# Optimization experiments

Hardware: AMD Instinct MI355X
Metric: run time of the kernel (lower is better)

The kernel has to match this reference:

```python
import jax, jax.numpy as jnp
import numpy as np

HID = 1024
HEADS = 16
HEAD_DIM = HID // HEADS
SCALE = np.sqrt(HEAD_DIM).astype(np.float32)


def setup_inputs() -> dict:
    key = jax.random.key(0)
    ks = jax.random.split(key, 13)
    B, S = 4, 2048
    inp = {
        'query': jax.random.normal(ks[0], (B, S, HID), jnp.float32),
        'key': jax.random.normal(ks[1], (B, S, HID), jnp.float32),
        'value': jax.random.normal(ks[2], (B, S, HID), jnp.float32),
        'mask': jax.random.randint(ks[3], (B, 1, 1, S), 0, 2, jnp.int32),
        'Wq': jax.random.normal(ks[4], (HID, HID), jnp.float32) / np.sqrt(HID),
        'bq': jax.random.normal(ks[5], (HID,), jnp.float32) * 0.02,
        'Wk': jax.random.normal(ks[6], (HID, HID), jnp.float32) / np.sqrt(HID),
        'bk': jax.random.normal(ks[7], (HID,), jnp.float32) * 0.02,
        'Wv': jax.random.normal(ks[8], (HID, HID), jnp.float32) / np.sqrt(HID),
        'bv': jax.random.normal(ks[9], (HID,), jnp.float32) * 0.02,
        'Wo': jax.random.normal(ks[10], (HID, HID), jnp.float32) / np.sqrt(HID),
        'bo': jax.random.normal(ks[11], (HID,), jnp.float32) * 0.02,
    }
    return inp


def reference(query, key, value, mask, Wq, bq, Wk, bk, Wv, bv, Wo, bo):
    B, Sq, _ = query.shape
    # nn.Linear: x @ W.T + b
    Q = (query @ Wq.T + bq).reshape(B, Sq, HEADS, HEAD_DIM)
    K = (key @ Wk.T + bk).reshape(B, -1, HEADS, HEAD_DIM)
    V = (value @ Wv.T + bv).reshape(B, -1, HEADS, HEAD_DIM)
    # energy: [B, H, Q, K]
    energy = jnp.einsum('bqnh,bknh->bnqk', Q, K) / SCALE
    energy = jnp.where(mask == 0, jnp.float32(-1e10), energy)
    attention = jax.nn.softmax(energy, axis=-1)  # dropout p=0.0 -> identity
    x = jnp.einsum('bnqk,bknh->bqnh', attention, V).reshape(B, Sq, HID)
    return x @ Wo.T + bo
```

## Files before the change

kernel.cpp:

```cpp
#include <hip/hip_runtime.h>
#include <cstddef>
#include <math.h>

#define S_LEN  2048
#define HID_C  1024
#define NHEADS 16
#define HDIM   64

typedef __attribute__((ext_vector_type(8))) short bf16x8;
typedef __attribute__((ext_vector_type(4))) float f32x4;
typedef __attribute__((ext_vector_type(16))) float f32x16;
typedef unsigned short ushort_t;

#define LOG2E 1.44269504088896f

__device__ __forceinline__ unsigned short f32_to_bf16_rn(float f) {
    unsigned int u = __float_as_uint(f);
    return (unsigned short)((u + 0x8000u) >> 16);
}

__device__ __forceinline__ float fexp2(float x) {
    float r;
    asm("v_exp_f32 %0, %1" : "=v"(r) : "v"(x));
    return r;
}

__device__ __forceinline__ void gload16(const ushort_t* g, ushort_t* l) {
    __builtin_amdgcn_global_load_lds(
        (const __attribute__((address_space(1))) void*)g,
        (__attribute__((address_space(3))) void*)l, 16, 0, 0);
}

__device__ __forceinline__ float tmax16(const f32x16& v) {
    float a0 = fmaxf(v[0], v[1]),   a1 = fmaxf(v[2], v[3]);
    float a2 = fmaxf(v[4], v[5]),   a3 = fmaxf(v[6], v[7]);
    float a4 = fmaxf(v[8], v[9]),   a5 = fmaxf(v[10], v[11]);
    float a6 = fmaxf(v[12], v[13]), a7 = fmaxf(v[14], v[15]);
    float b0 = fmaxf(a0, a1), b1 = fmaxf(a2, a3);
    float b2 = fmaxf(a4, a5), b3 = fmaxf(a6, a7);
    return fmaxf(fmaxf(b0, b1), fmaxf(b2, b3));
}
__device__ __forceinline__ float tsum16(const f32x16& v) {
    float a0 = v[0] + v[1],   a1 = v[2] + v[3];
    float a2 = v[4] + v[5],   a3 = v[6] + v[7];
    float a4 = v[8] + v[9],   a5 = v[10] + v[11];
    float a6 = v[12] + v[13], a7 = v[14] + v[15];
    float b0 = a0 + a1, b1 = a2 + a3, b2 = a4 + a5, b3 = a6 + a7;
    return (b0 + b1) + (b2 + b3);
}

__global__ void scan_mask(const int* __restrict__ mask, int* __restrict__ cidx,
                          int* __restrict__ nvalid, int* __restrict__ npads) {
    const int b = blockIdx.x;
    const int lane = threadIdx.x;
    int base = 0;
    for (int i = 0; i < S_LEN / 64; ++i) {
        const int s = i * 64 + lane;
        const int v = mask[b * S_LEN + s];
        const unsigned long long bal = __ballot(v != 0);
        const int pre = __popcll(bal & ((1ull << lane) - 1ull));
        if (v) cidx[b * S_LEN + base + pre] = s;
        base += (int)__popcll(bal);
    }
    if (lane == 0) { nvalid[b] = base; npads[b] = (base + 63) & ~63; }
}

#define CONVB 12288

__global__ void prep_gather(
    const float* __restrict__ query,
    const float* __restrict__ Wq, const float* __restrict__ Wk,
    const float* __restrict__ Wo, const float* __restrict__ Wv,
    const float* __restrict__ key, const float* __restrict__ value,
    const int* __restrict__ cidx, const int* __restrict__ nvalid,
    ushort_t* __restrict__ Qbf, ushort_t* __restrict__ Wqb,
    ushort_t* __restrict__ Wkb, ushort_t* __restrict__ Wob,
    ushort_t* __restrict__ Wvb,
    ushort_t* __restrict__ Kc, ushort_t* __restrict__ Vc,
    float* __restrict__ Mbc)
{
    if (blockIdx.x < CONVB) {
        const unsigned SEG = 4u * S_LEN * HID_C;
        const unsigned NW = HID_C * HID_C;
        unsigned i = (blockIdx.x * 256u + threadIdx.x) * 4u;
        const float* src; ushort_t* dst;
        if (i < SEG) { src = query; dst = Qbf; }
        else {
            i -= SEG;
            if (i < NW) { src = Wq; dst = Wqb; }
            else { i -= NW;
                if (i < NW) { src = Wk; dst = Wkb; }
                else { i -= NW;
                    if (i < NW) { src = Wo; dst = Wob; }
                    else { i -= NW; if (i >= NW) return; src = Wv; dst = Wvb; }
                }
            }
        }
        float4 v = *reinterpret_cast<const float4*>(src + i);
        uint2 p;
        p.x = ((unsigned)f32_to_bf16_rn(v.y) << 16) | f32_to_bf16_rn(v.x);
        p.y = ((unsigned)f32_to_bf16_rn(v.w) << 16) | f32_to_bf16_rn(v.z);
        *reinterpret_cast<uint2*>(dst + i) = p;
    } else {
        const int r = blockIdx.x - CONVB;
        const int b = r >> 11, j = r & 2047;
        const int tid = threadIdx.x;
        const int nv = nvalid[b];
        if (tid == 0) Mbc[r] = (j < nv) ? 0.f : -1e30f;
        const int np128 = (nv + 127) & ~127;
        if (j >= np128) return;
        uint2* kd = reinterpret_cast<uint2*>(Kc + (size_t)r * HID_C + tid * 4);
        uint2* vd = reinterpret_cast<uint2*>(Vc + (size_t)r * HID_C + tid * 4);
        if (j < nv) {
            const int src = cidx[b * S_LEN + j];
            const float4 kv = *reinterpret_cast<const float4*>(
                key + ((size_t)b * S_LEN + src) * HID_C + tid * 4);
            const float4 vv = *reinterpret_cast<const float4*>(
                value + ((size_t)b * S_LEN + src) * HID_C + tid * 4);
            uint2 kp, vp;
            kp.x = ((unsigned)f32_to_bf16_rn(kv.y) << 16) | f32_to_bf16_rn(kv.x);
            kp.y = ((unsigned)f32_to_bf16_rn(kv.w) << 16) | f32_to_bf16_rn(kv.z);
            vp.x = ((unsigned)f32_to_bf16_rn(vv.y) << 16) | f32_to_bf16_rn(vv.x);
            vp.y = ((unsigned)f32_to_bf16_rn(vv.w) << 16) | f32_to_bf16_rn(vv.z);
            *kd = kp; *vd = vp;
        } else {
            *kd = make_uint2(0u, 0u); *vd = make_uint2(0u, 0u);
        }
    }
}

__device__ __forceinline__ void gemm_core(
    const ushort_t* __restrict__ Ab, const ushort_t* __restrict__ Wb,
    const float* __restrict__ bias, ushort_t* __restrict__ outB,
    int bm, int bn, int N, int K, float oscale, bool rowBias,
    ushort_t* Ah, ushort_t* Bh)
{
    const int tid  = threadIdx.x;
    const int lane = tid & 63;
    const int wave = tid >> 6;
    const int wm = (wave >> 1) * 64;
    const int wn = (wave & 1) * 64;
    const int fr = lane & 15;
    const int kq = lane >> 4;

    int srow[2], skq[2];
#pragma unroll
    for (int i = 0; i < 2; ++i) {
        const int s = i * 256 + tid;
        srow[i] = s >> 2;
        skq[i] = (s & 3) ^ ((s >> 3) & 3);
    }
    const int wslot = tid & 192;

    f32x4 acc[4][4];
#pragma unroll
    for (int i = 0; i < 4; ++i)
#pragma unroll
        for (int j = 0; j < 4; ++j)
#pragma unroll
            for (int r = 0; r < 4; ++r) acc[i][j][r] = 0.f;

    for (int k0 = 0; k0 < K; k0 += 32) {
        __syncthreads();
#pragma unroll
        for (int i = 0; i < 2; ++i) {
            const int sb = (i * 256 + wslot) * 8;
            gload16(Ab + (size_t)(bm + srow[i]) * K + k0 + skq[i] * 8, Ah + sb);
            gload16(Wb + (size_t)(bn + srow[i]) * K + k0 + skq[i] * 8, Bh + sb);
        }
        __syncthreads();

        bf16x8 fah[4], fbh[4];
#pragma unroll
        for (int mi = 0; mi < 4; ++mi) {
            const int rr = wm + mi * 16 + fr;
            fah[mi] = *reinterpret_cast<const bf16x8*>(
                Ah + (rr * 4 + (kq ^ ((rr >> 1) & 3))) * 8);
        }
#pragma unroll
        for (int ni = 0; ni < 4; ++ni) {
            const int rr = wn + ni * 16 + fr;
            fbh[ni] = *reinterpret_cast<const bf16x8*>(
                Bh + (rr * 4 + (kq ^ ((rr >> 1) & 3))) * 8);
        }

#pragma unroll
        for (int mi = 0; mi < 4; ++mi)
#pragma unroll
            for (int ni = 0; ni < 4; ++ni)
                acc[mi][ni] = __builtin_amdgcn_mfma_f32_16x16x32_bf16(
                    fah[mi], fbh[ni], acc[mi][ni], 0, 0, 0);
    }

    const int fq = lane >> 4;
    if (rowBias) {
#pragma unroll
        for (int mi = 0; mi < 4; ++mi)
#pragma unroll
            for (int r = 0; r < 4; ++r) {
                const int row = bm + wm + mi * 16 + fq * 4 + r;
                const float bvr = bias[row];
#pragma unroll
                for (int ni = 0; ni < 4; ++ni)
                    outB[(size_t)row * N + bn + wn + ni * 16 + fr] =
                        f32_to_bf16_rn((acc[mi][ni][r] + bvr) * oscale);
            }
    } else {
        float bv[4];
#pragma unroll
        for (int ni = 0; ni < 4; ++ni) bv[ni] = bias[bn + wn + ni * 16 + fr];
#pragma unroll
        for (int mi = 0; mi < 4; ++mi)
#pragma unroll
            for (int ni = 0; ni < 4; ++ni) {
                const size_t rowb = (size_t)(bm + wm + mi * 16 + fq * 4);
                const int col = bn + wn + ni * 16 + fr;
#pragma unroll
                for (int r = 0; r < 4; ++r)
                    outB[(rowb + r) * N + col] =
                        f32_to_bf16_rn((acc[mi][ni][r] + bv[ni]) * oscale);
            }
    }
}

__global__ __launch_bounds__(256) void proj_fused(
    const ushort_t* __restrict__ Qbf, const ushort_t* __restrict__ Kc,
    const ushort_t* __restrict__ Wvb, const ushort_t* __restrict__ Vc,
    const ushort_t* __restrict__ Wqb, const ushort_t* __restrict__ Wkb,
    const float* __restrict__ bq, const float* __restrict__ bk,
    const float* __restrict__ bv, const int* __restrict__ npads,
    ushort_t* __restrict__ Qb, ushort_t* __restrict__ Kb,
    ushort_t* __restrict__ Vtg, float sc2)
{
    __shared__ __align__(16) ushort_t Ah[128 * 32];
    __shared__ __align__(16) ushort_t Bh[128 * 32];

    int id = blockIdx.x;
    if (id < 512) {
        gemm_core(Qbf, Wqb, bq, Qb, (id >> 3) * 128, (id & 7) * 128,
                  HID_C, HID_C, sc2, false, Ah, Bh);
    } else if (id < 1024) {
        id -= 512;
        const int bm = (id >> 3) * 128;
        if ((bm & 2047) >= npads[bm >> 11]) return;
        gemm_core(Kc, Wkb, bk, Kb, bm, (id & 7) * 128,
                  HID_C, HID_C, 1.f, false, Ah, Bh);
    } else {
        id -= 1024;
        const int bn = (id & 63) * 128;
        if ((bn & 2047) >= npads[bn >> 11]) return;
        gemm_core(Wvb, Vc, bv, Vtg, (id >> 6) * 128, bn,
                  4 * S_LEN, HID_C, 1.f, true, Ah, Bh);
    }
}

__global__ __launch_bounds__(256) void gemm_out(
    const ushort_t* __restrict__ Xhi, const ushort_t* __restrict__ Xlo,
    const ushort_t* __restrict__ Wb, const float* __restrict__ bias,
    float* __restrict__ outF, int M, int N, int K)
{
    __shared__ __align__(16) ushort_t Ah[128 * 32];
    __shared__ __align__(16) ushort_t Al[128 * 32];
    __shared__ __align__(16) ushort_t Bh[128 * 32];

    const int tid  = threadIdx.x;
    const int lane = tid & 63;
    const int wave = tid >> 6;
    const int bm = blockIdx.y * 128;
    const int bn = blockIdx.x * 128;
    const int wm = (wave >> 1) * 64;
    const int wn = (wave & 1) * 64;
    const int fr = lane & 15;
    const int kq = lane >> 4;

    int srow[2], skq[2];
#pragma unroll
    for (int i = 0; i < 2; ++i) {
        const int s = i * 256 + tid;
        srow[i] = s >> 2;
        skq[i] = (s & 3) ^ ((s >> 3) & 3);
    }
    const int wslot = tid & 192;

    f32x4 acc[4][4];
#pragma unroll
    for (int i = 0; i < 4; ++i)
#pragma unroll
        for (int j = 0; j < 4; ++j)
#pragma unroll
            for (int r = 0; r < 4; ++r) acc[i][j][r] = 0.f;

    for (int k0 = 0; k0 < K; k0 += 32) {
        __syncthreads();
#pragma unroll
        for (int i = 0; i < 2; ++i) {
            const int sb = (i * 256 + wslot) * 8;
            const size_t ga = (size_t)(bm + srow[i]) * K + k0 + skq[i] * 8;
            gload16(Xhi + ga, Ah + sb);
            gload16(Xlo + ga, Al + sb);
            gload16(Wb + (size_t)(bn + srow[i]) * K + k0 + skq[i] * 8, Bh + sb);
        }
        __syncthreads();

        bf16x8 fah[4], fal[4], fbh[4];
#pragma unroll
        for (int mi = 0; mi < 4; ++mi) {
            const int rr = wm + mi * 16 + fr;
            const int sl = (rr * 4 + (kq ^ ((rr >> 1) & 3))) * 8;
            fah[mi] = *reinterpret_cast<const bf16x8*>(Ah + sl);
            fal[mi] = *reinterpret_cast<const bf16x8*>(Al + sl);
        }
#pragma unroll
        for (int ni = 0; ni < 4; ++ni) {
            const int rr = wn + ni * 16 + fr;
            fbh[ni] = *reinterpret_cast<const bf16x8*>(
                Bh + (rr * 4 + (kq ^ ((rr >> 1) & 3))) * 8);
        }

#pragma unroll
        for (int mi = 0; mi < 4; ++mi)
#pragma unroll
            for (int ni = 0; ni < 4; ++ni) {
                acc[mi][ni] = __builtin_amdgcn_mfma_f32_16x16x32_bf16(
                    fah[mi], fbh[ni], acc[mi][ni], 0, 0, 0);
                acc[mi][ni] = __builtin_amdgcn_mfma_f32_16x16x32_bf16(
                    fal[mi], fbh[ni], acc[mi][ni], 0, 0, 0);
            }
    }

    const int fq = lane >> 4;
    float bv[4];
#pragma unroll
    for (int ni = 0; ni < 4; ++ni) bv[ni] = bias[bn + wn + ni * 16 + fr];
#pragma unroll
    for (int mi = 0; mi < 4; ++mi)
#pragma unroll
        for (int ni = 0; ni < 4; ++ni) {
            const size_t rowb = (size_t)(bm + wm + mi * 16 + fq * 4);
            const int col = bn + wn + ni * 16 + fr;
#pragma unroll
            for (int r = 0; r < 4; ++r)
                outF[(rowb + r) * N + col] = acc[mi][ni][r] + bv[ni];
        }
}

#define QBLK 128
#define KVB  64
#define LDA  72

__global__ __launch_bounds__(256) void flash_attn_bf16(
    const ushort_t* __restrict__ Qb, const ushort_t* __restrict__ Kb,
    const ushort_t* __restrict__ Vtg, const float* __restrict__ maskb,
    const int* __restrict__ npads,
    ushort_t* __restrict__ Xhi, ushort_t* __restrict__ Xlo)
{
    __shared__ __align__(16) ushort_t Ks[KVB * LDA];
    __shared__ __align__(16) ushort_t Vt[HDIM * LDA];
    __shared__ float Xpose[QBLK];

    const int n  = blockIdx.x;
    const int bh = (n & 7) * 8 + ((n >> 3) & 7);
    const int qx = n >> 6;
    const int b  = bh >> 4;
    const int h  = bh & 15;
    const int q0 = qx * QBLK;

    const int tid  = threadIdx.x;
    const int lane = tid & 63;
    const int w    = tid >> 6;
    const int lq = lane & 31;
    const int lh = lane >> 5;

    const size_t bS = (size_t)b * S_LEN;
    const int hc = h * HDIM;
    const int npad = npads[b];

    bf16x8 qf[4];
#pragma unroll
    for (int s = 0; s < 4; ++s)
        qf[s] = *reinterpret_cast<const bf16x8*>(
            &Qb[(bS + q0 + w * 32 + lq) * HID_C + hc + s * 16 + lh * 8]);

    f32x16 OV[2], zc;
#pragma unroll
    for (int r = 0; r < 16; ++r) { OV[0][r] = 0.f; OV[1][r] = 0.f; zc[r] = 0.f; }
    float m_ = -1e30f, l_ = 0.f;

    const int sr  = tid >> 2;
    const int seg = tid & 3;
    const ushort_t* kbase = &Kb[(bS + sr) * HID_C + hc + seg * 16];
    const ushort_t* vbase = &Vtg[(size_t)(hc + sr) * (4 * S_LEN) + bS + seg * 16];

    {
        bf16x8 kv0 = *reinterpret_cast<const bf16x8*>(kbase);
        bf16x8 kv1 = *reinterpret_cast<const bf16x8*>(kbase + 8);
        bf16x8 vv0 = *reinterpret_cast<const bf16x8*>(vbase);
        bf16x8 vv1 = *reinterpret_cast<const bf16x8*>(vbase + 8);
        *reinterpret_cast<bf16x8*>(&Ks[sr * LDA + seg * 16])     = kv0;
        *reinterpret_cast<bf16x8*>(&Ks[sr * LDA + seg * 16 + 8]) = kv1;
        *reinterpret_cast<bf16x8*>(&Vt[sr * LDA + seg * 16])     = vv0;
        *reinterpret_cast<bf16x8*>(&Vt[sr * LDA + seg * 16 + 8]) = vv1;
        __syncthreads();
    }

    for (int t = 0; t < npad; t += KVB) {
        f32x16 S[2];
        __builtin_amdgcn_s_setprio(1);
#pragma unroll
        for (int kt = 0; kt < 2; ++kt) {
            bf16x8 kf0 = *reinterpret_cast<const bf16x8*>(
                &Ks[(kt * 32 + lq) * LDA + lh * 8]);
            S[kt] = __builtin_amdgcn_mfma_f32_32x32x16_bf16(kf0, qf[0], zc, 0, 0, 0);
#pragma unroll
            for (int s = 1; s < 4; ++s) {
                bf16x8 kf = *reinterpret_cast<const bf16x8*>(
                    &Ks[(kt * 32 + lq) * LDA + s * 16 + lh * 8]);
                S[kt] = __builtin_amdgcn_mfma_f32_32x32x16_bf16(
                    kf, qf[s], S[kt], 0, 0, 0);
            }
        }
        __builtin_amdgcn_s_setprio(0);

        const bool more = (t + KVB < npad);
        bf16x8 kv0n, kv1n, vv0n, vv1n;
        if (more) {
            const ushort_t* kp = kbase + (size_t)(t + KVB) * HID_C;
            const ushort_t* vp = vbase + (t + KVB);
            kv0n = *reinterpret_cast<const bf16x8*>(kp);
            kv1n = *reinterpret_cast<const bf16x8*>(kp + 8);
            vv0n = *reinterpret_cast<const bf16x8*>(vp);
            vv1n = *reinterpret_cast<const bf16x8*>(vp + 8);
        }

        if (!more) {
#pragma unroll
            for (int kt = 0; kt < 2; ++kt)
#pragma unroll
                for (int g = 0; g < 4; ++g) {
                    float4 mv = *reinterpret_cast<const float4*>(
                        &maskb[bS + t + kt * 32 + g * 8 + lh * 4]);
#pragma unroll
                    for (int e = 0; e < 4; ++e)
                        S[kt][g * 4 + e] += reinterpret_cast<const float*>(&mv)[e];
                }
        }

        float mx = fmaxf(tmax16(S[0]), tmax16(S[1]));
        mx = fmaxf(mx, __shfl_xor(mx, 32));

        if (!__all(mx <= m_ + 8.f)) {
            float mn = fmaxf(m_, mx);
            float corr = fexp2(m_ - mn);
            m_ = mn; l_ *= corr;
            if (lh == 0) Xpose[w * 32 + lq] = corr;
#pragma unroll
            for (int r = 0; r < 16; ++r) {
                float cq = Xpose[w * 32 + (r & 3) + 8 * (r >> 2) + 4 * lh];
                OV[0][r] *= cq;
                OV[1][r] *= cq;
            }
        }

#pragma unroll
        for (int kt = 0; kt < 2; ++kt)
#pragma unroll
            for (int r = 0; r < 16; ++r) S[kt][r] = fexp2(S[kt][r] - m_);
        float ls = tsum16(S[0]) + tsum16(S[1]);
        ls += __shfl_xor(ls, 32);
        l_ += ls;

        bf16x8 pa[4];
#pragma unroll
        for (int kt = 0; kt < 2; ++kt)
#pragma unroll
            for (int u = 0; u < 2; ++u) {
                const int bb = u * 8;
                unsigned int c0, c1, c2, c3;
                asm("v_cvt_pk_bf16_f32 %0, %1, %2"
                    : "=v"(c0) : "v"(S[kt][bb + 0]), "v"(S[kt][bb + 1]));
                asm("v_cvt_pk_bf16_f32 %0, %1, %2"
                    : "=v"(c1) : "v"(S[kt][bb + 2]), "v"(S[kt][bb + 3]));
                asm("v_cvt_pk_bf16_f32 %0, %1, %2"
                    : "=v"(c2) : "v"(S[kt][bb + 4]), "v"(S[kt][bb + 5]));
                asm("v_cvt_pk_bf16_f32 %0, %1, %2"
                    : "=v"(c3) : "v"(S[kt][bb + 6]), "v"(S[kt][bb + 7]));
                asm("v_permlane32_swap_b32 %0, %1" : "+v"(c0), "+v"(c2));
                asm("v_permlane32_swap_b32 %0, %1" : "+v"(c1), "+v"(c3));
                uint4 wv = make_uint4(c0, c1, c2, c3);
                pa[kt * 2 + u] = *reinterpret_cast<bf16x8*>(&wv);
            }

        __builtin_amdgcn_s_setprio(1);
#pragma unroll
        for (int dt = 0; dt < 2; ++dt)
#pragma unroll
            for (int f = 0; f < 4; ++f) {
                bf16x8 vf = *reinterpret_cast<const bf16x8*>(
                    &Vt[(dt * 32 + lq) * LDA + f * 16 + lh * 8]);
                OV[dt] = __builtin_amdgcn_mfma_f32_32x32x16_bf16(
                    pa[f], vf, OV[dt], 0, 0, 0);
            }
        __builtin_amdgcn_s_setprio(0);

        __syncthreads();
        if (more) {
            *reinterpret_cast<bf16x8*>(&Ks[sr * LDA + seg * 16])     = kv0n;
            *reinterpret_cast<bf16x8*>(&Ks[sr * LDA + seg * 16 + 8]) = kv1n;
            *reinterpret_cast<bf16x8*>(&Vt[sr * LDA + seg * 16])     = vv0n;
            *reinterpret_cast<bf16x8*>(&Vt[sr * LDA + seg * 16 + 8]) = vv1n;
            __syncthreads();
        }
    }

    if (lh == 0) Xpose[w * 32 + lq] = 1.f / l_;
#pragma unroll
    for (int r = 0; r < 16; ++r) {
        const int qr = (r & 3) + 8 * (r >> 2) + 4 * lh;
        const float inv = Xpose[w * 32 + qr];
        const size_t row = bS + q0 + w * 32 + qr;
#pragma unroll
        for (int dt = 0; dt < 2; ++dt) {
            float v = OV[dt][r] * inv;
            unsigned int u = __float_as_uint(v);
            unsigned short hi = (unsigned short)(u >> 16);
            float res = v - __uint_as_float(u & 0xFFFF0000u);
            Xhi[row * HID_C + hc + dt * 32 + lq] = hi;
            Xlo[row * HID_C + hc + dt * 32 + lq] = f32_to_bf16_rn(res);
        }
    }
}

extern "C" void kernel_launch(void* const* d_in, const int* in_sizes, int n_in,
                              void* d_out, int out_size, void* d_ws, size_t ws_size,
                              hipStream_t stream) {
    const float* query = (const float*)d_in[0];
    const float* key   = (const float*)d_in[1];
    const float* value = (const float*)d_in[2];
    const int*   mask  = (const int*)d_in[3];
    const float* Wq = (const float*)d_in[4];
    const float* bq = (const float*)d_in[5];
    const float* Wk = (const float*)d_in[6];
    const float* bk = (const float*)d_in[7];
    const float* Wv = (const float*)d_in[8];
    const float* bv = (const float*)d_in[9];
    const float* Wo = (const float*)d_in[10];
    const float* bo = (const float*)d_in[11];
    float* out = (float*)d_out;

    const int B = 4, M = B * S_LEN;
    const size_t seg = (size_t)M * HID_C;
    const size_t nw  = (size_t)HID_C * HID_C;

    ushort_t* Qb  = (ushort_t*)d_ws;
    ushort_t* Kb  = Qb + seg;
    ushort_t* Vtg = Kb + seg;
    ushort_t* Xhi = Vtg + seg;
    ushort_t* Xlo = Xhi + seg;
    ushort_t* Qbf = Xlo + seg;
    float*    Mbc = (float*)(Qbf + seg);
    ushort_t* Wqb = (ushort_t*)(Mbc + 4 * S_LEN);
    ushort_t* Wkb = Wqb + nw;
    ushort_t* Wob = Wkb + nw;
    ushort_t* Wvb = Wob + nw;
    int*      cidx   = (int*)(Wvb + nw);
    int*      nvalid = cidx + 4 * S_LEN;
    int*      npads  = nvalid + 4;

    ushort_t* Kc = Xhi;
    ushort_t* Vc = Xlo;

    scan_mask<<<dim3(4), 64, 0, stream>>>(mask, cidx, nvalid, npads);
    prep_gather<<<dim3(CONVB + M), 256, 0, stream>>>(
        query, Wq, Wk, Wo, Wv, key, value, cidx, nvalid,
        Qbf, Wqb, Wkb, Wob, Wvb, Kc, Vc, Mbc);

    const float SC2 = 0.125f * LOG2E;
    proj_fused<<<dim3(1536), 256, 0, stream>>>(
        Qbf, Kc, Wvb, Vc, Wqb, Wkb, bq, bk, bv, npads, Qb, Kb, Vtg, SC2);

    flash_attn_bf16<<<dim3((S_LEN / QBLK) * B * NHEADS), 256, 0, stream>>>(
        Qb, Kb, Vtg, Mbc, npads, Xhi, Xlo);

    gemm_out<<<dim3(HID_C / 128, M / 128), 256, 0, stream>>>(
        Xhi, Xlo, Wob, bo, out, M, HID_C, HID_C);
}
```

Baseline: 199.2 us.

## Double-buffer K/V tiles with direct global-to-LDS loads and XOR swizzle

The flash attention loop now stages K and V^T tiles into two LDS buffers using gload16 (direct global-to-LDS transfers), issuing the next tile's loads at the start of each iteration so they overlap the current QK and PV MFMAs. The padded LDA=72 layout is replaced by an XOR-swizzled 8-chunk layout to avoid bank conflicts. This removes the register staging and the second barrier per iteration. In exchange it doubles LDS use and relies on the single end-of-loop barrier to order the async loads correctly.

New measurement: 206.5 us. +3.7%, slower.

```diff
diff --git a/kernel.cpp b/kernel.cpp
--- a/kernel.cpp
+++ b/kernel.cpp
@@ -346,7 +346,6 @@
 
 #define QBLK 128
 #define KVB  64
-#define LDA  72
 
 __global__ __launch_bounds__(256) void flash_attn_bf16(
     const ushort_t* __restrict__ Qb, const ushort_t* __restrict__ Kb,
@@ -354,8 +353,8 @@
     const int* __restrict__ npads,
     ushort_t* __restrict__ Xhi, ushort_t* __restrict__ Xlo)
 {
-    __shared__ __align__(16) ushort_t Ks[KVB * LDA];
-    __shared__ __align__(16) ushort_t Vt[HDIM * LDA];
+    __shared__ __align__(16) ushort_t Ks[2][512 * 8];
+    __shared__ __align__(16) ushort_t Vt[2][512 * 8];
     __shared__ float Xpose[QBLK];
 
     const int n  = blockIdx.x;
@@ -386,51 +385,61 @@
     for (int r = 0; r < 16; ++r) { OV[0][r] = 0.f; OV[1][r] = 0.f; zc[r] = 0.f; }
     float m_ = -1e30f, l_ = 0.f;
 
-    const int sr  = tid >> 2;
-    const int seg = tid & 3;
-    const ushort_t* kbase = &Kb[(bS + sr) * HID_C + hc + seg * 16];
-    const ushort_t* vbase = &Vtg[(size_t)(hc + sr) * (4 * S_LEN) + bS + seg * 16];
-
-    {
-        bf16x8 kv0 = *reinterpret_cast<const bf16x8*>(kbase);
-        bf16x8 kv1 = *reinterpret_cast<const bf16x8*>(kbase + 8);
-        bf16x8 vv0 = *reinterpret_cast<const bf16x8*>(vbase);
-        bf16x8 vv1 = *reinterpret_cast<const bf16x8*>(vbase + 8);
-        *reinterpret_cast<bf16x8*>(&Ks[sr * LDA + seg * 16])     = kv0;
-        *reinterpret_cast<bf16x8*>(&Ks[sr * LDA + seg * 16 + 8]) = kv1;
-        *reinterpret_cast<bf16x8*>(&Vt[sr * LDA + seg * 16])     = vv0;
-        *reinterpret_cast<bf16x8*>(&Vt[sr * LDA + seg * 16 + 8]) = vv1;
-        __syncthreads();
-    }
+    const int wslot = tid & 192;
+    int srow[2], schk[2];
+#pragma unroll
+    for (int i = 0; i < 2; ++i) {
+        const int s = i * 256 + tid;
+        srow[i] = s >> 3;
+        schk[i] = (s & 7) ^ ((s >> 3) & 7);
+    }
+    const ushort_t* ksrc[2];
+    const ushort_t* vsrc[2];
+#pragma unroll
+    for (int i = 0; i < 2; ++i) {
+        ksrc[i] = Kb + (bS + srow[i]) * HID_C + hc + schk[i] * 8;
+        vsrc[i] = Vtg + (size_t)(hc + srow[i]) * (4 * S_LEN) + bS + schk[i] * 8;
+    }
+
+#pragma unroll
+    for (int i = 0; i < 2; ++i) {
+        const int sb = (i * 256 + wslot) * 8;
+        gload16(ksrc[i], &Ks[0][sb]);
+        gload16(vsrc[i], &Vt[0][sb]);
+    }
+    __syncthreads();
 
     for (int t = 0; t < npad; t += KVB) {
+        const int  cur  = (t >> 6) & 1;
+        const bool more = (t + KVB < npad);
+
+        if (more) {
+#pragma unroll
+            for (int i = 0; i < 2; ++i) {
+                const int sb = (i * 256 + wslot) * 8;
+                gload16(ksrc[i] + (size_t)(t + KVB) * HID_C, &Ks[cur ^ 1][sb]);
+                gload16(vsrc[i] + (t + KVB),                 &Vt[cur ^ 1][sb]);
+            }
+        }
+
         f32x16 S[2];
         __builtin_amdgcn_s_setprio(1);
 #pragma unroll
         for (int kt = 0; kt < 2; ++kt) {
+            const int row = kt * 32 + lq;
+            const int rx  = row & 7;
             bf16x8 kf0 = *reinterpret_cast<const bf16x8*>(
-                &Ks[(kt * 32 + lq) * LDA + lh * 8]);
+                &Ks[cur][(row * 8 + (lh ^ rx)) * 8]);
             S[kt] = __builtin_amdgcn_mfma_f32_32x32x16_bf16(kf0, qf[0], zc, 0, 0, 0);
 #pragma unroll
             for (int s = 1; s < 4; ++s) {
                 bf16x8 kf = *reinterpret_cast<const bf16x8*>(
-                    &Ks[(kt * 32 + lq) * LDA + s * 16 + lh * 8]);
+                    &Ks[cur][(row * 8 + ((s * 2 + lh) ^ rx)) * 8]);
                 S[kt] = __builtin_amdgcn_mfma_f32_32x32x16_bf16(
                     kf, qf[s], S[kt], 0, 0, 0);
             }
         }
         __builtin_amdgcn_s_setprio(0);
-
-        const bool more = (t + KVB < npad);
-        bf16x8 kv0n, kv1n, vv0n, vv1n;
-        if (more) {
-            const ushort_t* kp = kbase + (size_t)(t + KVB) * HID_C;
-            const ushort_t* vp = vbase + (t + KVB);
-            kv0n = *reinterpret_cast<const bf16x8*>(kp);
-            kv1n = *reinterpret_cast<const bf16x8*>(kp + 8);
-            vv0n = *reinterpret_cast<const bf16x8*>(vp);
-            vv1n = *reinterpret_cast<const bf16x8*>(vp + 8);
-        }
 
         if (!more) {
 #pragma unroll
@@ -492,24 +501,20 @@
 
         __builtin_amdgcn_s_setprio(1);
 #pragma unroll
-        for (int dt = 0; dt < 2; ++dt)
+        for (int dt = 0; dt < 2; ++dt) {
+            const int row = dt * 32 + lq;
+            const int rx  = row & 7;
 #pragma unroll
             for (int f = 0; f < 4; ++f) {
                 bf16x8 vf = *reinterpret_cast<const bf16x8*>(
-                    &Vt[(dt * 32 + lq) * LDA + f * 16 + lh * 8]);
+                    &Vt[cur][(row * 8 + ((f * 2 + lh) ^ rx)) * 8]);
                 OV[dt] = __builtin_amdgcn_mfma_f32_32x32x16_bf16(
                     pa[f], vf, OV[dt], 0, 0, 0);
             }
+        }
         __builtin_amdgcn_s_setprio(0);
 
         __syncthreads();
-        if (more) {
-            *reinterpret_cast<bf16x8*>(&Ks[sr * LDA + seg * 16])     = kv0n;
-            *reinterpret_cast<bf16x8*>(&Ks[sr * LDA + seg * 16 + 8]) = kv1n;
-            *reinterpret_cast<bf16x8*>(&Vt[sr * LDA + seg * 16])     = vv0n;
-            *reinterpret_cast<bf16x8*>(&Vt[sr * LDA + seg * 16 + 8]) = vv1n;
-            __syncthreads();
-        }
     }
 
     if (lh == 0) Xpose[w * 32 + lq] = 1.f / l_;
```
